# Kernel tuning notes

Measured on AMD Instinct MI355X. Metric: run time of the kernel, lower is better.

Reference implementation:

```python
import jax, jax.numpy as jnp
import numpy as np

B, T, HID = 2, 1024, 768
EXPAND, NH, HD, NG, NS, K = 2, 24, 64, 1, 128, 4
INTER = EXPAND * HID            # 1536
CONV_DIM = INTER + 2 * NG * NS  # 1792
NLVL = 15                       # get_num_levels(16384, base=2)
EPS = 1e-5


def _levels(T):
    # Fenwick-style hierarchical level matrix (HType.WEAK, base 2):
    # level(t, s) = 0 on the diagonal, else msb(t XOR s) + 1.
    t = np.arange(T)
    x = t[:, None] ^ t[None, :]
    lev = np.zeros((T, T), np.int32)
    nz = x > 0
    lev[nz] = np.floor(np.log2(x[nz])).astype(np.int32) + 1
    return lev

_LEV = jnp.asarray(_levels(T))  # [T,T] int32, values in [0, NLVL)


def setup_inputs() -> dict:
    key = jax.random.key(0)
    ks = jax.random.split(key, 4)
    P = INTER + CONV_DIM + NH * (NLVL + 1)  # 3712
    return {
        "hidden_states": jax.random.normal(ks[0], (B, T, HID), jnp.float32),
        "in_proj_w": jax.random.normal(ks[1], (P, HID), jnp.float32) * (HID ** -0.5),
        "conv_w": jax.random.normal(ks[2], (CONV_DIM, 1, K), jnp.float32) * 0.2,
        "conv_b": jnp.zeros((CONV_DIM,), jnp.float32),
        "dt_bias": jnp.ones((NH,), jnp.float32),
        "A_log": jnp.log(jnp.arange(1, NH + 1, dtype=jnp.float32)),
        "L": jnp.ones((NH, NLVL), jnp.float32),
        "D": jnp.ones((NH,), jnp.float32),
        "norm_weight": jnp.ones((INTER,), jnp.float32),
        "out_proj_w": jax.random.normal(ks[3], (HID, INTER), jnp.float32) * (INTER ** -0.5),
    }


def reference(hidden_states, in_proj_w, conv_w, conv_b, dt_bias, A_log, L, D,
              norm_weight, out_proj_w):
    # in_proj and split: [gate | xBC | dt | dl]
    proj = hidden_states @ in_proj_w.T                       # [B,T,P]
    gate = proj[..., :INTER]
    xBC = proj[..., INTER:INTER + CONV_DIM]
    dt = proj[..., INTER + CONV_DIM:INTER + CONV_DIM + NH]
    dl = proj[..., INTER + CONV_DIM + NH:].reshape(B, T, NH, NLVL)

    # fused causal depthwise conv1d + SiLU
    xBC = jax.lax.conv_general_dilated(
        xBC.transpose(0, 2, 1), conv_w, window_strides=(1,),
        padding=[(K - 1, 0)], dimension_numbers=("NCH", "OIH", "NCH"),
        feature_group_count=CONV_DIM) + conv_b[None, :, None]
    xBC = jax.nn.silu(xBC.transpose(0, 2, 1))                # [B,T,CONV_DIM]

    x = xBC[..., :INTER].reshape(B, T, NH, HD)               # [B,T,H,P]
    Bm = xBC[..., INTER:INTER + NG * NS].reshape(B, T, NG, NS)
    Cm = xBC[..., INTER + NG * NS:].reshape(B, T, NG, NS)
    hpg = NH // NG
    Bh = jnp.repeat(Bm, hpg, axis=2)                         # [B,T,H,N]
    Ch = jnp.repeat(Cm, hpg, axis=2)

    dt = jax.nn.softplus(dt + dt_bias)                       # [B,T,H]
    A = -jnp.exp(A_log)                                      # [H]
    cumA = jnp.cumsum(dt * A, axis=1)                        # [B,T,H]

    # semiseparable decay exp(sum_{s<r<=t} dt_r * A), causal-masked
    cA = cumA.transpose(0, 2, 1)                             # [B,H,T]
    diff = cA[:, :, :, None] - cA[:, :, None, :]             # [B,H,T,T]
    mask = jnp.tril(jnp.ones((T, T), bool))
    decay = jnp.exp(jnp.where(mask[None, None], diff, -1e9))

    CB = jnp.einsum("bthn,bshn->bhts", Ch, Bh)               # [B,H,T,T]

    # hierarchical lambda gating: positive lambda, per-head learned scale L
    lam = jax.nn.softplus(dl) * L                            # [B,T,H,NLVL]
    lam_g = jnp.take_along_axis(lam.transpose(0, 2, 1, 3),
                                _LEV[None, None], axis=-1)   # [B,H,T,T]

    M = CB * decay * lam_g * dt.transpose(0, 2, 1)[:, :, None, :]
    y = jnp.einsum("bhts,bshp->bthp", M, x)                  # [B,T,H,P]
    y = y + D[None, None, :, None] * x
    y = y.reshape(B, T, INTER)

    # gated RMSNorm (norm_before_gate=False): norm(y * silu(gate))
    y = y * jax.nn.silu(gate)
    var = jnp.mean(jnp.square(y), axis=-1, keepdims=True)
    y = y * jax.lax.rsqrt(var + EPS) * norm_weight

    return y @ out_proj_w.T                                  # [B,T,HID]
```

## Files before the change

kernel.cpp:

```cpp
#include <hip/hip_runtime.h>
#include <hip/hip_bf16.h>
#include <math.h>

#define B_ 2
#define T_ 1024
#define HID_ 768
#define INTER_ 1536
#define NH_ 24
#define HD_ 64
#define NS_ 128
#define NLVL_ 15
#define CONV_DIM_ 1792
#define P_ 3712
#define EPS_ 1e-5f

typedef short short8_t __attribute__((ext_vector_type(8)));
typedef short short4_t __attribute__((ext_vector_type(4)));
typedef float float4_t __attribute__((ext_vector_type(4)));


__device__ __forceinline__ float softplus_f(float x) {
  return (x > 20.f) ? x : log1pf(__expf(x));
}
__device__ __forceinline__ short f2bf(float f) {
  union { float f; unsigned u; } v; v.f = f;
  unsigned r = v.u + 0x7FFF + ((v.u >> 16) & 1);
  return (short)(r >> 16);
}
__device__ __forceinline__ float bf2f(short s) {
  union { unsigned u; float f; } v; v.u = ((unsigned)(unsigned short)s) << 16;
  return v.f;
}
__device__ __forceinline__ void gl_lds16(const void* g, void* l) {
  __builtin_amdgcn_global_load_lds(
      (const __attribute__((address_space(1))) unsigned int*)g,
      (__attribute__((address_space(3))) unsigned int*)l, 16, 0, 0);
}

__global__ __launch_bounds__(256) void cvtdt_k(
    const float* __restrict__ hs, const float* __restrict__ Win, const float* __restrict__ Wout,
    short* __restrict__ hsbf, short* __restrict__ wibf, short* __restrict__ wobf,
    float* __restrict__ dtraw, int ncvt)
{
  const long na = (long)B_ * T_ * HID_, nb = (long)P_ * HID_, nc = (long)HID_ * INTER_;
  if ((int)blockIdx.x < ncvt) {
    const long i = ((long)blockIdx.x * 256 + threadIdx.x) * 8;
    const float* src; short* dst; long off;
    if (i < na)           { src = hs;   dst = hsbf; off = i; }
    else if (i < na + nb) { src = Win;  dst = wibf; off = i - na; }
    else if (i < na + nb + nc) { src = Wout; dst = wobf; off = i - na - nb; }
    else return;
    const long base = (off & ~31L) + ((off >> 3) & 3) * 4;
    float4 v0 = *(const float4*)(src + base);
    float4 v1 = *(const float4*)(src + base + 16);
    short8_t o;
    o[0] = f2bf(v0.x); o[1] = f2bf(v0.y); o[2] = f2bf(v0.z); o[3] = f2bf(v0.w);
    o[4] = f2bf(v1.x); o[5] = f2bf(v1.y); o[6] = f2bf(v1.z); o[7] = f2bf(v1.w);
    *(short8_t*)(dst + off) = o;
  } else {
    const int rowbt = ((int)blockIdx.x - ncvt) * 4 + (threadIdx.x >> 6);
    const int lane = threadIdx.x & 63;
    float hv[12];
    const float* hrow = hs + (long)rowbt * HID_ + lane * 12;
    #pragma unroll
    for (int j = 0; j < 12; j++) hv[j] = hrow[j];
    const float* wbase = Win + (long)(INTER_ + CONV_DIM_) * HID_ + lane * 12;
    for (int h = 0; h < NH_; h++) {
      const float* wr = wbase + (long)h * HID_;
      float s = 0.f;
      #pragma unroll
      for (int j = 0; j < 12; j++) s = fmaf(hv[j], wr[j], s);
      #pragma unroll
      for (int off = 32; off; off >>= 1) s += __shfl_xor(s, off);
      if (lane == 0) dtraw[(long)rowbt * NH_ + h] = s;
    }
  }
}

__device__ __forceinline__ short8_t ldfrag(const short* Ts, int row, int lg) {
  return *(const short8_t*)(Ts + row * 32 + lg * 8);
}

__device__ __forceinline__ short8_t ldfrag64(const short* Ts, int row, int kk, int lg) {
  const int cc = (kk * 4 + lg) ^ (row & 7);
  return *(const short8_t*)(Ts + row * 64 + cc * 8);
}

__global__ __launch_bounds__(256) void inproj_scan_k(
    const short* __restrict__ A, const short* __restrict__ B, short* __restrict__ C,
    const float* __restrict__ dtraw, const float* __restrict__ dt_bias,
    const float* __restrict__ A_log, float* __restrict__ dtT, float* __restrict__ cAT,
    float* __restrict__ qT)
{
  constexpr int TM = 128, TN = 128, K = HID_, BK = 64;
  constexpr int PSZ = TM * 32;
  constexpr int ASZ = 2 * PSZ;
  __shared__ short As[2 * ASZ];
  __shared__ short Bs[2 * ASZ];

  if (blockIdx.y >= 16) {
    const int sid = ((int)blockIdx.y - 16) * 29 + (int)blockIdx.x;
    if (sid >= B_ * NH_) return;
    const int b = sid / NH_;
    const int h = sid % NH_;
    const float bias = dt_bias[h];
    const float Ah = -__expf(A_log[h]);
    const long ob = (long)(h * B_ + b) * T_;
    float* sc = (float*)As;
    float carry = 0.f;
    for (int c0 = 0; c0 < T_; c0 += 256) {
      const int t = c0 + threadIdx.x;
      const long bt = (long)b * T_ + t;
      float sp = softplus_f(dtraw[bt * NH_ + h] + bias);
      dtT[ob + t] = sp;
      sc[threadIdx.x] = sp * Ah;
      __syncthreads();
      for (int off = 1; off < 256; off <<= 1) {
        float add = (threadIdx.x >= off) ? sc[threadIdx.x - off] : 0.f;
        __syncthreads();
        sc[threadIdx.x] += add;
        __syncthreads();
      }
      cAT[ob + t] = carry + sc[threadIdx.x];
      qT[ob + t] = sp * __expf(sc[threadIdx.x | 63] - sc[threadIdx.x]);
      float tot = sc[255];
      __syncthreads();
      carry += tot;
    }
    return;
  }

  const int tid = threadIdx.x;
  const int w = tid >> 6, lane = tid & 63;
  const int lr = lane & 15, lg = lane >> 4;
  const int wr = w >> 1, wc = w & 1;
  const int m0 = blockIdx.y * TM, n0 = blockIdx.x * TN;
  const int srow = lane >> 2;
  const int sc2 = (lane & 3) * 8;

  auto stage = [&](int buf, int k0) {
    #pragma unroll
    for (int it = 0; it < 2; it++) {
      const int cb = w + 4 * it;
      const int row = cb * 16 + srow;
      #pragma unroll
      for (int kg = 0; kg < 2; kg++) {
        gl_lds16(A + (long)(m0 + row) * K + k0 + kg * 32 + sc2,
                 As + buf * ASZ + kg * PSZ + cb * 512);
        gl_lds16(B + (long)(n0 + row) * K + k0 + kg * 32 + sc2,
                 Bs + buf * ASZ + kg * PSZ + cb * 512);
      }
    }
  };

  float4_t acc[4][4] = {};
  int cur = 0;
  stage(0, 0);
  for (int k0 = 0; k0 < K; k0 += BK) {
    __syncthreads();
    if (k0 + BK < K) stage(cur ^ 1, k0 + BK);
    #pragma unroll
    for (int kg = 0; kg < 2; kg++) {
      const short* Ab = As + cur * ASZ + kg * PSZ;
      const short* Bb = Bs + cur * ASZ + kg * PSZ;
      short8_t af[4], bf[4];
      #pragma unroll
      for (int m = 0; m < 4; m++) af[m] = ldfrag(Ab, wr * 64 + m * 16 + lr, lg);
      #pragma unroll
      for (int n = 0; n < 4; n++) bf[n] = ldfrag(Bb, wc * 64 + n * 16 + lr, lg);
      #pragma unroll
      for (int m = 0; m < 4; m++)
        #pragma unroll
        for (int n = 0; n < 4; n++)
          acc[m][n] = __builtin_amdgcn_mfma_f32_16x16x32_bf16(af[m], bf[n], acc[m][n], 0, 0, 0);
    }
    cur ^= 1;
  }

  #pragma unroll
  for (int m = 0; m < 4; m++)
    #pragma unroll
    for (int n = 0; n < 4; n++)
      #pragma unroll
      for (int r = 0; r < 4; r++) {
        const int row = m0 + wr * 64 + m * 16 + lg * 4 + r;
        const int col = n0 + wc * 64 + n * 16 + lr;
        C[(long)row * P_ + col] = f2bf(acc[m][n][r]);
      }
}

__global__ __launch_bounds__(256) void gemm_out_k(
    const short* __restrict__ A, const short* __restrict__ B, float* __restrict__ C,
    int M, int N, int K)
{
  constexpr int PSZ = 64 * 32;
  constexpr int BKG = 4;
  constexpr int BUF = PSZ * BKG;
  __shared__ short As[2 * BUF];
  __shared__ short Bs[2 * BUF];
  const int tid = threadIdx.x;
  const int w = tid >> 6, lane = tid & 63;
  const int lr = lane & 15, lg = lane >> 4;
  const int wr = w >> 1, wc = w & 1;
  const int m0 = blockIdx.y * 64, n0 = blockIdx.x * 64;
  const int srow = lane >> 2;
  const int sc = (lane & 3) * 8;

  auto stage = [&](int buf, int k0) {
    const int row = w * 16 + srow;
    #pragma unroll
    for (int kg = 0; kg < BKG; kg++) {
      gl_lds16(A + (long)(m0 + row) * K + k0 + kg * 32 + sc, As + buf * BUF + kg * PSZ + w * 512);
      gl_lds16(B + (long)(n0 + row) * K + k0 + kg * 32 + sc, Bs + buf * BUF + kg * PSZ + w * 512);
    }
  };

  float4_t acc[2][2] = {};
  int cur = 0;
  stage(0, 0);
  for (int k0 = 0; k0 < K; k0 += 128) {
    __syncthreads();
    if (k0 + 128 < K) stage(cur ^ 1, k0 + 128);
    #pragma unroll
    for (int kg = 0; kg < BKG; kg++) {
      const short* Ab = As + cur * BUF + kg * PSZ;
      const short* Bb = Bs + cur * BUF + kg * PSZ;
      short8_t af[2], bf[2];
      #pragma unroll
      for (int m = 0; m < 2; m++) af[m] = ldfrag(Ab, wr * 32 + m * 16 + lr, lg);
      #pragma unroll
      for (int n = 0; n < 2; n++) bf[n] = ldfrag(Bb, wc * 32 + n * 16 + lr, lg);
      #pragma unroll
      for (int m = 0; m < 2; m++)
        #pragma unroll
        for (int n = 0; n < 2; n++)
          acc[m][n] = __builtin_amdgcn_mfma_f32_16x16x32_bf16(af[m], bf[n], acc[m][n], 0, 0, 0);
    }
    cur ^= 1;
  }

  #pragma unroll
  for (int m = 0; m < 2; m++)
    #pragma unroll
    for (int n = 0; n < 2; n++)
      #pragma unroll
      for (int r = 0; r < 4; r++) {
        const int row = m0 + wr * 32 + m * 16 + lg * 4 + r;
        const int col = n0 + wc * 32 + n * 16 + lr;
        C[(long)row * N + col] = acc[m][n][r];
      }
}

__global__ __launch_bounds__(256) void gemm_cbh_k(
    const short* __restrict__ Chh, const short* __restrict__ Bh, short* __restrict__ CBh)
{
  if (blockIdx.x > blockIdx.y) return;
  Chh += (long)blockIdx.z * T_ * NS_;
  Bh  += (long)blockIdx.z * T_ * NS_;
  CBh += (long)blockIdx.z * T_ * T_;
  constexpr int PSZ = 64 * 32;
  __shared__ short As[4 * PSZ];
  __shared__ short Bs[4 * PSZ];
  const int tid = threadIdx.x;
  const int w = tid >> 6, lane = tid & 63;
  const int lr = lane & 15, lg = lane >> 4;
  const int wr = w >> 1, wc = w & 1;
  const int m0 = blockIdx.y * 64, n0 = blockIdx.x * 64;
  const int srow = lane >> 2;
  const int sc = (lane & 3) * 8;

  {
    const int row = w * 16 + srow;
    #pragma unroll
    for (int kg = 0; kg < 4; kg++) {
      gl_lds16(Chh + (long)(m0 + row) * NS_ + kg * 32 + sc, As + kg * PSZ + w * 512);
      gl_lds16(Bh  + (long)(n0 + row) * NS_ + kg * 32 + sc, Bs + kg * PSZ + w * 512);
    }
  }
  __syncthreads();

  float4_t acc[2][2] = {};
  #pragma unroll
  for (int kg = 0; kg < 4; kg++) {
    const short* Ab = As + kg * PSZ;
    const short* Bb = Bs + kg * PSZ;
    short8_t af[2], bf[2];
    #pragma unroll
    for (int m = 0; m < 2; m++) af[m] = ldfrag(Ab, wr * 32 + m * 16 + lr, lg);
    #pragma unroll
    for (int n = 0; n < 2; n++) bf[n] = ldfrag(Bb, wc * 32 + n * 16 + lr, lg);
    #pragma unroll
    for (int m = 0; m < 2; m++)
      #pragma unroll
      for (int n = 0; n < 2; n++)
        acc[m][n] = __builtin_amdgcn_mfma_f32_16x16x32_bf16(af[m], bf[n], acc[m][n], 0, 0, 0);
  }

  #pragma unroll
  for (int m = 0; m < 2; m++)
    #pragma unroll
    for (int n = 0; n < 2; n++)
      #pragma unroll
      for (int r = 0; r < 4; r++) {
        const int row = m0 + wr * 32 + m * 16 + lg * 4 + r;
        const int sl = wc * 32 + n * 16 + lr;
        const int g = sl >> 5, k32 = sl & 31;
        const int cc = g * 4 + ((k32 >> 2) & 3);
        const int off = ((cc ^ (row & 7)) * 8) + 4 * (k32 >> 4) + (k32 & 3);
        CBh[(long)row * T_ + n0 + off] = f2bf(acc[m][n][r]);
      }
}

__global__ __launch_bounds__(256) void conv_silu_k(
    const short* __restrict__ projh, const float* __restrict__ cw, const float* __restrict__ cbias,
    const float* __restrict__ qT,
    short* __restrict__ xTr, short* __restrict__ xTq,
    short* __restrict__ Bh, short* __restrict__ Chh)
{
  const int c0 = blockIdx.x * 256;
  const int t0 = blockIdx.y * 16;
  const int b  = blockIdx.z;
  const int tid = threadIdx.x;
  __shared__ float S[19][256];
  for (int q = tid; q < 19 * 32; q += 256) {
    const int r = q >> 5, c8 = (q & 31) * 8;
    const int t = t0 - 3 + r;
    float4 f0 = {0.f, 0.f, 0.f, 0.f}, f1 = {0.f, 0.f, 0.f, 0.f};
    if (t >= 0) {
      short8_t v = *(const short8_t*)(projh + ((long)b * T_ + t) * P_ + INTER_ + c0 + c8);
      f0.x = bf2f(v[0]); f0.y = bf2f(v[1]); f0.z = bf2f(v[2]); f0.w = bf2f(v[3]);
      f1.x = bf2f(v[4]); f1.y = bf2f(v[5]); f1.z = bf2f(v[6]); f1.w = bf2f(v[7]);
    }
    *(float4*)(&S[r][c8])     = f0;
    *(float4*)(&S[r][c8 + 4]) = f1;
  }
  __syncthreads();
  const int c = c0 + tid;
  const float4 w = *(const float4*)(cw + c * 4);
  const float bias = cbias[c];
  float acc[16];
  #pragma unroll
  for (int tt = 0; tt < 16; tt++) {
    float a = bias + w.w * S[tt + 3][tid] + w.z * S[tt + 2][tid]
                   + w.y * S[tt + 1][tid] + w.x * S[tt][tid];
    acc[tt] = a / (1.f + __expf(-a));
  }
  if (c < INTER_) {
    const int h = c >> 6, hd = c & 63;
    const long chb = (long)(h * B_ + b) * T_;
    float qv[16];
    #pragma unroll
    for (int qq = 0; qq < 4; qq++) {
      float4 q4 = *(const float4*)(qT + chb + t0 + qq * 4);
      qv[qq*4+0] = q4.x; qv[qq*4+1] = q4.y; qv[qq*4+2] = q4.z; qv[qq*4+3] = q4.w;
    }
    const long base = ((long)(b * NH_ + h) * HD_ + hd) * T_ + (t0 & ~63);
    const int g = (t0 >> 5) & 1, h2 = (t0 >> 4) & 1, sw = hd & 7;
    #pragma unroll
    for (int a = 0; a < 4; a++) {
      short4_t xr, xq;
      #pragma unroll
      for (int r = 0; r < 4; r++) {
        xr[r] = f2bf(acc[a * 4 + r]);
        xq[r] = f2bf(acc[a * 4 + r] * qv[a * 4 + r]);
      }
      const int off = (((g * 4 + a) ^ sw) * 8) + h2 * 4;
      *(short4_t*)(xTr + base + off) = xr;
      *(short4_t*)(xTq + base + off) = xq;
    }
  } else {
    const int ch0 = c - INTER_;
    const bool isB = ch0 < NS_;
    const int k = isB ? ch0 : ch0 - NS_;
    const int k32 = k & 31;
    const int P = (k & ~31) + 8 * ((k32 >> 2) & 3) + 4 * (k32 >> 4) + (k32 & 3);
    short* dst = isB ? Bh : Chh;
    #pragma unroll
    for (int tt = 0; tt < 16; tt++) {
      const long bt = (long)b * T_ + t0 + tt;
      dst[bt * NS_ + P] = f2bf(acc[tt]);
    }
  }
}

__global__ __launch_bounds__(256) void attn_mfma3_k(
    const short* __restrict__ xTr, const short* __restrict__ xTq,
    const short* __restrict__ CBh,
    const float* __restrict__ cAT, const float* __restrict__ dtT,
    const short* __restrict__ projh, const float* __restrict__ Lw,
    const float* __restrict__ Dv,
    short* __restrict__ ybh)
{
  const int h = blockIdx.x;
  const int tt = (T_ / 64 - 1) - blockIdx.y;
  const int b = blockIdx.z;
  const int t0 = tt * 64;
  const int tid = threadIdx.x;
  const int w = tid >> 6, lane = tid & 63;
  const int lr = lane & 15, lg = lane >> 4;

  __shared__ short CBl[3][64 * 64];
  __shared__ short Xl[3][64 * 64];
  __shared__ float lamS[64][17];
  __shared__ float caEs[16];

  const long chb = (long)(h * B_ + b) * T_;
  for (int f = tid; f < 64 * NLVL_; f += 256) {
    int r = f / NLVL_, l = f - r * NLVL_;
    lamS[r][l] = softplus_f(
        bf2f(projh[((long)b * T_ + t0 + r) * P_ + INTER_ + CONV_DIM_ + NH_ + h * NLVL_ + l]))
        * Lw[h * NLVL_ + l];
  }
  if (tid < 16) caEs[tid] = cAT[chb + tid * 64 + 63];

  const int tl = w * 16 + lr;
  const int t  = t0 + tl;
  const int orow = w * 16 + lg * 4;
  const float catv = cAT[chb + t];
  float cao[4];
  #pragma unroll
  for (int r = 0; r < 4; r++) cao[r] = cAT[chb + t0 + orow + r];

  const short* xbr = xTr + (long)(b * NH_ + h) * HD_ * T_;
  const short* xbq = xTq + (long)(b * NH_ + h) * HD_ * T_;
  const short* CBbase = CBh + (long)b * T_ * T_ + (long)t0 * T_;

  const int srow = w * 16 + (lane >> 3);
  const int sch = (lane & 7) * 8;

  auto stage = [&](int buf, int st) {
    const int s0 = st * 64;
    const short* xsrc = (st == tt) ? xbr : xbq;
    #pragma unroll
    for (int i = 0; i < 2; i++) {
      gl_lds16(CBbase + (long)(srow + i * 8) * T_ + s0 + sch, &CBl[buf][(w * 16 + i * 8) * 64]);
      gl_lds16(xsrc + (long)(srow + i * 8) * T_ + s0 + sch, &Xl[buf][(w * 16 + i * 8) * 64]);
    }
  };

  float4_t acc[4] = {};
  stage(0, 0);
  if (tt >= 1) stage(1, 1);
  asm volatile("s_waitcnt lgkmcnt(0)" ::: "memory");

  for (int st = 0; st <= tt; st++) {
    if (st < tt) asm volatile("s_waitcnt vmcnt(4)" ::: "memory");
    else         asm volatile("s_waitcnt vmcnt(0)" ::: "memory");
    __builtin_amdgcn_s_barrier();
    __builtin_amdgcn_sched_barrier(0);
    if (st + 2 <= tt) stage((st + 2) % 3, st + 2);
    const int cur = st % 3;
    const int s0 = st * 64;
    if (st < tt) {
      const float caE = caEs[st];
      const int lev = 32 - __clz(t0 ^ s0);
      float k1o[4];
      #pragma unroll
      for (int r = 0; r < 4; r++)
        k1o[r] = __expf(cao[r] - caE) * lamS[orow + r][lev];
      float4_t dtile[4] = {};
      __builtin_amdgcn_s_setprio(1);
      #pragma unroll
      for (int kk = 0; kk < 2; kk++) {
        short8_t af = ldfrag64(CBl[cur], tl, kk, lg);
        #pragma unroll
        for (int n = 0; n < 4; n++) {
          short8_t bfv = ldfrag64(Xl[cur], n * 16 + lr, kk, lg);
          dtile[n] = __builtin_amdgcn_mfma_f32_16x16x32_bf16(af, bfv, dtile[n], 0, 0, 0);
        }
      }
      __builtin_amdgcn_s_setprio(0);
      #pragma unroll
      for (int n = 0; n < 4; n++)
        #pragma unroll
        for (int r = 0; r < 4; r++)
          acc[n][r] = fmaf(k1o[r], dtile[n][r], acc[n][r]);
    } else {
      #pragma unroll
      for (int kk = 0; kk < 2; kk++) {
        short8_t cb8 = ldfrag64(CBl[cur], tl, kk, lg);
        short8_t af;
        #pragma unroll
        for (int g = 0; g < 2; g++) {
          const int sb = s0 + kk * 32 + g * 16 + lg * 4;
          float4_t ca4 = *(const float4_t*)(cAT + chb + sb);
          float4_t dt4 = *(const float4_t*)(dtT + chb + sb);
          #pragma unroll
          for (int a = 0; a < 4; a++) {
            const int sg = sb + a;
            float m = 0.f;
            if (sg <= t) {
              const int xo = t ^ sg;
              const int lev2 = xo ? (32 - __clz(xo)) : 0;
              m = bf2f(cb8[g * 4 + a]) * __expf(catv - ca4[a]) * lamS[tl][lev2] * dt4[a];
            }
            af[g * 4 + a] = f2bf(m);
          }
        }
        __builtin_amdgcn_s_setprio(1);
        #pragma unroll
        for (int n = 0; n < 4; n++) {
          short8_t bfv = ldfrag64(Xl[cur], n * 16 + lr, kk, lg);
          acc[n] = __builtin_amdgcn_mfma_f32_16x16x32_bf16(af, bfv, acc[n], 0, 0, 0);
        }
        __builtin_amdgcn_s_setprio(0);
      }
    }
  }

  const float Dh = Dv[h];
  const short* Xd = Xl[tt % 3];
  #pragma unroll
  for (int n = 0; n < 4; n++) {
    #pragma unroll
    for (int r = 0; r < 4; r++) {
      const int trow = t0 + orow + r;
      const int hd = n * 16 + lr;
      const int xoff = hd * 64 + ((((w >> 1) * 4 + lg) ^ (hd & 7)) * 8) + (w & 1) * 4 + r;
      const float xv = bf2f(Xd[xoff]);
      ybh[((long)b * T_ + trow) * INTER_ + h * HD_ + hd] = f2bf(acc[n][r] + Dh * xv);
    }
  }
}

__global__ __launch_bounds__(192) void gate_rms_k(
    const short* __restrict__ ybh, const short* __restrict__ projh,
    const float* __restrict__ nw, short* __restrict__ ynorm)
{
  const long bt = blockIdx.x;
  const short* gp = projh + bt * P_;
  const short* yp = ybh + bt * INTER_;
  const int i = threadIdx.x;
  const int lo = (i >> 2) * 32 + (i & 3) * 4;
  const int hi = lo + 16;
  float v[8];
  float ss = 0.f;
  {
    short4_t g0 = *(const short4_t*)(gp + lo);
    short4_t g1 = *(const short4_t*)(gp + hi);
    short4_t y0 = *(const short4_t*)(yp + lo);
    short4_t y1 = *(const short4_t*)(yp + hi);
    float ga[8] = {bf2f(g0[0]), bf2f(g0[1]), bf2f(g0[2]), bf2f(g0[3]),
                   bf2f(g1[0]), bf2f(g1[1]), bf2f(g1[2]), bf2f(g1[3])};
    float ya[8] = {bf2f(y0[0]), bf2f(y0[1]), bf2f(y0[2]), bf2f(y0[3]),
                   bf2f(y1[0]), bf2f(y1[1]), bf2f(y1[2]), bf2f(y1[3])};
    #pragma unroll
    for (int j = 0; j < 8; j++) {
      float val = ya[j] * (ga[j] / (1.f + __expf(-ga[j])));
      v[j] = val;
      ss += val * val;
    }
  }
  #pragma unroll
  for (int off = 32; off > 0; off >>= 1) ss += __shfl_xor(ss, off);
  __shared__ float part[3];
  if ((i & 63) == 0) part[i >> 6] = ss;
  __syncthreads();
  const float tot = part[0] + part[1] + part[2];
  const float r = rsqrtf(tot * (1.f / INTER_) + EPS_);
  short8_t o;
  #pragma unroll
  for (int j = 0; j < 8; j++) {
    const int idx = (j < 4) ? (lo + j) : (hi + j - 4);
    o[j] = f2bf(v[j] * r * nw[idx]);
  }
  *(short8_t*)(ynorm + bt * INTER_ + i * 8) = o;
}

extern "C" void kernel_launch(void* const* d_in, const int* in_sizes, int n_in,
                              void* d_out, int out_size, void* d_ws, size_t ws_size,
                              hipStream_t stream) {
  const float* hs   = (const float*)d_in[0];
  const float* Win  = (const float*)d_in[1];
  const float* cw   = (const float*)d_in[2];
  const float* cb   = (const float*)d_in[3];
  const float* dtb  = (const float*)d_in[4];
  const float* Alog = (const float*)d_in[5];
  const float* Lw   = (const float*)d_in[6];
  const float* Dv   = (const float*)d_in[7];
  const float* nw   = (const float*)d_in[8];
  const float* Wout = (const float*)d_in[9];
  float* out = (float*)d_out;

  const long n_hs = (long)B_ * T_ * HID_;
  const long n_wi = (long)P_ * HID_;
  const long n_wo = (long)HID_ * INTER_;

  float* ws = (float*)d_ws;
  long o = 0;
  float* projreg = ws + o; o += (long)B_ * T_ * P_ / 2 + 16;
  short* xbf   = (short*)(ws + o); o += (long)B_ * T_ * INTER_ / 2;
  short* Bh    = (short*)(ws + o); o += (long)B_ * T_ * NS_ / 2;
  short* Chh   = (short*)(ws + o); o += (long)B_ * T_ * NS_ / 2;
  float* dtT   = ws + o; o += (long)B_ * T_ * NH_;
  float* cAT   = ws + o; o += (long)B_ * T_ * NH_;
  float* qT    = ws + o; o += (long)B_ * T_ * NH_;
  float* dtraw = ws + o; o += (long)B_ * T_ * NH_;
  short* CBh   = (short*)(ws + o); o += (long)B_ * T_ * T_ / 2;
  short* ybh   = (short*)(ws + o); o += (long)B_ * T_ * INTER_ / 2;
  float* yxreg = ws + o; o += (long)B_ * T_ * INTER_ / 2;
  short* hsbf  = (short*)(ws + o); o += n_hs / 2;
  short* wibf  = (short*)(ws + o); o += n_wi / 2;
  short* wobf  = (short*)(ws + o); o += n_wo / 2;
  short* projh = (short*)projreg;
  short* xTr   = (short*)yxreg;
  short* ynrmb = (short*)yxreg;
  short* xTq   = hsbf;
  (void)xbf;

  const int ncvt = (int)((n_hs + n_wi + n_wo) / 8 / 256);

  cvtdt_k<<<ncvt + (B_ * T_) / 4, 256, 0, stream>>>(
      hs, Win, Wout, hsbf, wibf, wobf, dtraw, ncvt);
  inproj_scan_k<<<dim3(P_ / 128, 18), 256, 0, stream>>>(
      hsbf, wibf, projh, dtraw, dtb, Alog, dtT, cAT, qT);
  conv_silu_k<<<dim3(CONV_DIM_ / 256, T_ / 16, B_), 256, 0, stream>>>(
      projh, cw, cb, qT, xTr, xTq, Bh, Chh);
  gemm_cbh_k<<<dim3(T_ / 64, T_ / 64, B_), 256, 0, stream>>>(Chh, Bh, CBh);
  attn_mfma3_k<<<dim3(NH_, T_ / 64, B_), 256, 0, stream>>>(
      xTr, xTq, CBh, cAT, dtT, projh, Lw, Dv, ybh);
  gate_rms_k<<<B_ * T_, 192, 0, stream>>>(ybh, projh, nw, ynrmb);
  gemm_out_k<<<dim3(HID_ / 64, (B_ * T_) / 64), 256, 0, stream>>>(
      ynrmb, wobf, out, B_ * T_, HID_, INTER_);
}
```

Baseline: 107.4 us.

## Switch in-proj and out-proj GEMMs to three-stage LDS pipeline with partial waitcnt

Both the in-projection GEMM and the output GEMM move from double buffering with a full __syncthreads per K-step to a triple-buffered ring. Each step issues the load two steps ahead and waits with s_waitcnt vmcnt(4), so the newest stage's loads stay in flight. The K-step shrinks (32 for in_proj, 64 for out_proj), which means more barriers but less shared memory per stage. MFMA blocks are also wrapped in s_setprio raises. The risk is that the hand-picked vmcnt value must match the number of outstanding loads per stage.

```diff
diff --git a/kernel.cpp b/kernel.cpp
--- a/kernel.cpp
+++ b/kernel.cpp
@@ -92,11 +92,11 @@
     const float* __restrict__ A_log, float* __restrict__ dtT, float* __restrict__ cAT,
     float* __restrict__ qT)
 {
-  constexpr int TM = 128, TN = 128, K = HID_, BK = 64;
+  constexpr int TM = 128, TN = 128, K = HID_;
   constexpr int PSZ = TM * 32;
-  constexpr int ASZ = 2 * PSZ;
-  __shared__ short As[2 * ASZ];
-  __shared__ short Bs[2 * ASZ];
+  constexpr int NSTEP = K / 32;
+  __shared__ short As[3 * PSZ];
+  __shared__ short Bs[3 * PSZ];
 
   if (blockIdx.y >= 16) {
     const int sid = ((int)blockIdx.y - 16) * 29 + (int)blockIdx.x;
@@ -143,38 +143,34 @@
     for (int it = 0; it < 2; it++) {
       const int cb = w + 4 * it;
       const int row = cb * 16 + srow;
-      #pragma unroll
-      for (int kg = 0; kg < 2; kg++) {
-        gl_lds16(A + (long)(m0 + row) * K + k0 + kg * 32 + sc2,
-                 As + buf * ASZ + kg * PSZ + cb * 512);
-        gl_lds16(B + (long)(n0 + row) * K + k0 + kg * 32 + sc2,
-                 Bs + buf * ASZ + kg * PSZ + cb * 512);
-      }
+      gl_lds16(A + (long)(m0 + row) * K + k0 + sc2, As + buf * PSZ + cb * 512);
+      gl_lds16(B + (long)(n0 + row) * K + k0 + sc2, Bs + buf * PSZ + cb * 512);
     }
   };
 
   float4_t acc[4][4] = {};
-  int cur = 0;
   stage(0, 0);
-  for (int k0 = 0; k0 < K; k0 += BK) {
-    __syncthreads();
-    if (k0 + BK < K) stage(cur ^ 1, k0 + BK);
-    #pragma unroll
-    for (int kg = 0; kg < 2; kg++) {
-      const short* Ab = As + cur * ASZ + kg * PSZ;
-      const short* Bb = Bs + cur * ASZ + kg * PSZ;
-      short8_t af[4], bf[4];
-      #pragma unroll
-      for (int m = 0; m < 4; m++) af[m] = ldfrag(Ab, wr * 64 + m * 16 + lr, lg);
-      #pragma unroll
-      for (int n = 0; n < 4; n++) bf[n] = ldfrag(Bb, wc * 64 + n * 16 + lr, lg);
-      #pragma unroll
-      for (int m = 0; m < 4; m++)
-        #pragma unroll
-        for (int n = 0; n < 4; n++)
-          acc[m][n] = __builtin_amdgcn_mfma_f32_16x16x32_bf16(af[m], bf[n], acc[m][n], 0, 0, 0);
-    }
-    cur ^= 1;
+  stage(1, 32);
+  for (int ks = 0; ks < NSTEP; ks++) {
+    if (ks < NSTEP - 1) asm volatile("s_waitcnt vmcnt(4)" ::: "memory");
+    else                asm volatile("s_waitcnt vmcnt(0)" ::: "memory");
+    __builtin_amdgcn_s_barrier();
+    __builtin_amdgcn_sched_barrier(0);
+    if (ks + 2 < NSTEP) stage((ks + 2) % 3, (ks + 2) * 32);
+    const short* Ab = As + (ks % 3) * PSZ;
+    const short* Bb = Bs + (ks % 3) * PSZ;
+    short8_t af[4], bf[4];
+    #pragma unroll
+    for (int m = 0; m < 4; m++) af[m] = ldfrag(Ab, wr * 64 + m * 16 + lr, lg);
+    #pragma unroll
+    for (int n = 0; n < 4; n++) bf[n] = ldfrag(Bb, wc * 64 + n * 16 + lr, lg);
+    __builtin_amdgcn_s_setprio(1);
+    #pragma unroll
+    for (int m = 0; m < 4; m++)
+      #pragma unroll
+      for (int n = 0; n < 4; n++)
+        acc[m][n] = __builtin_amdgcn_mfma_f32_16x16x32_bf16(af[m], bf[n], acc[m][n], 0, 0, 0);
+    __builtin_amdgcn_s_setprio(0);
   }
 
   #pragma unroll
@@ -194,10 +190,10 @@
     int M, int N, int K)
 {
   constexpr int PSZ = 64 * 32;
-  constexpr int BKG = 4;
+  constexpr int BKG = 2;
   constexpr int BUF = PSZ * BKG;
-  __shared__ short As[2 * BUF];
-  __shared__ short Bs[2 * BUF];
+  __shared__ short As[3 * BUF];
+  __shared__ short Bs[3 * BUF];
   const int tid = threadIdx.x;
   const int w = tid >> 6, lane = tid & 63;
   const int lr = lane & 15, lg = lane >> 4;
@@ -205,6 +201,7 @@
   const int m0 = blockIdx.y * 64, n0 = blockIdx.x * 64;
   const int srow = lane >> 2;
   const int sc = (lane & 3) * 8;
+  const int NSTEP = K / 64;
 
   auto stage = [&](int buf, int k0) {
     const int row = w * 16 + srow;
@@ -216,27 +213,31 @@
   };
 
   float4_t acc[2][2] = {};
-  int cur = 0;
   stage(0, 0);
-  for (int k0 = 0; k0 < K; k0 += 128) {
-    __syncthreads();
-    if (k0 + 128 < K) stage(cur ^ 1, k0 + 128);
+  stage(1, 64);
+  for (int ks = 0; ks < NSTEP; ks++) {
+    if (ks < NSTEP - 1) asm volatile("s_waitcnt vmcnt(4)" ::: "memory");
+    else                asm volatile("s_waitcnt vmcnt(0)" ::: "memory");
+    __builtin_amdgcn_s_barrier();
+    __builtin_amdgcn_sched_barrier(0);
+    if (ks + 2 < NSTEP) stage((ks + 2) % 3, (ks + 2) * 64);
     #pragma unroll
     for (int kg = 0; kg < BKG; kg++) {
-      const short* Ab = As + cur * BUF + kg * PSZ;
-      const short* Bb = Bs + cur * BUF + kg * PSZ;
+      const short* Ab = As + (ks % 3) * BUF + kg * PSZ;
+      const short* Bb = Bs + (ks % 3) * BUF + kg * PSZ;
       short8_t af[2], bf[2];
       #pragma unroll
       for (int m = 0; m < 2; m++) af[m] = ldfrag(Ab, wr * 32 + m * 16 + lr, lg);
       #pragma unroll
       for (int n = 0; n < 2; n++) bf[n] = ldfrag(Bb, wc * 32 + n * 16 + lr, lg);
+      __builtin_amdgcn_s_setprio(1);
       #pragma unroll
       for (int m = 0; m < 2; m++)
         #pragma unroll
         for (int n = 0; n < 2; n++)
           acc[m][n] = __builtin_amdgcn_mfma_f32_16x16x32_bf16(af[m], bf[n], acc[m][n], 0, 0, 0);
-    }
-    cur ^= 1;
+      __builtin_amdgcn_s_setprio(0);
+    }
   }
 
   #pragma unroll
```

Measured after the change: 112.6 us. 4.8% more time.

## Process two heads per attention block to reuse the shared CB tile

Applied to the files above, without the earlier changes.

Each attention workgroup now handles two heads instead of one. The CB tile is shared across heads because NG=1, so each CB tile staged into LDS serves twice the MFMA work, halving global CB traffic. The lambda table is transposed to a level-major layout. The trade-off is half as many workgroups, more LDS (extra X buffers) and more accumulator registers, which may lower occupancy and parallelism.

```diff
diff --git a/kernel.cpp b/kernel.cpp
--- a/kernel.cpp
+++ b/kernel.cpp
@@ -391,7 +391,7 @@
     const float* __restrict__ Dv,
     short* __restrict__ ybh)
 {
-  const int h = blockIdx.x;
+  const int h0 = blockIdx.x * 2;
   const int tt = (T_ / 64 - 1) - blockIdx.y;
   const int b = blockIdx.z;
   const int t0 = tt * 64;
@@ -400,29 +400,39 @@
   const int lr = lane & 15, lg = lane >> 4;
 
   __shared__ short CBl[3][64 * 64];
-  __shared__ short Xl[3][64 * 64];
-  __shared__ float lamS[64][17];
-  __shared__ float caEs[16];
-
-  const long chb = (long)(h * B_ + b) * T_;
-  for (int f = tid; f < 64 * NLVL_; f += 256) {
-    int r = f / NLVL_, l = f - r * NLVL_;
-    lamS[r][l] = softplus_f(
-        bf2f(projh[((long)b * T_ + t0 + r) * P_ + INTER_ + CONV_DIM_ + NH_ + h * NLVL_ + l]))
-        * Lw[h * NLVL_ + l];
-  }
-  if (tid < 16) caEs[tid] = cAT[chb + tid * 64 + 63];
+  __shared__ short Xl[2][3][64 * 64];
+  __shared__ float lamS[2][NLVL_ * 64];
+  __shared__ float caEs[2][16];
+
+  #pragma unroll 1
+  for (int f = tid; f < 2 * 64 * NLVL_; f += 256) {
+    const int hh = f / (64 * NLVL_);
+    const int rem = f - hh * 64 * NLVL_;
+    const int r = rem / NLVL_, l = rem - r * NLVL_;
+    lamS[hh][l * 64 + r] = softplus_f(
+        bf2f(projh[((long)b * T_ + t0 + r) * P_ + INTER_ + CONV_DIM_ + NH_ + (h0 + hh) * NLVL_ + l]))
+        * Lw[(h0 + hh) * NLVL_ + l];
+  }
+  if (tid < 32)
+    caEs[tid >> 4][tid & 15] =
+        cAT[(long)((h0 + (tid >> 4)) * B_ + b) * T_ + (tid & 15) * 64 + 63];
 
   const int tl = w * 16 + lr;
   const int t  = t0 + tl;
   const int orow = w * 16 + lg * 4;
-  const float catv = cAT[chb + t];
-  float cao[4];
-  #pragma unroll
-  for (int r = 0; r < 4; r++) cao[r] = cAT[chb + t0 + orow + r];
-
-  const short* xbr = xTr + (long)(b * NH_ + h) * HD_ * T_;
-  const short* xbq = xTq + (long)(b * NH_ + h) * HD_ * T_;
+
+  long chb[2]; float catv[2]; float cao[2][4];
+  const short *xbr[2], *xbq[2];
+  #pragma unroll
+  for (int hh = 0; hh < 2; hh++) {
+    const int h = h0 + hh;
+    chb[hh] = (long)(h * B_ + b) * T_;
+    catv[hh] = cAT[chb[hh] + t];
+    #pragma unroll
+    for (int r = 0; r < 4; r++) cao[hh][r] = cAT[chb[hh] + t0 + orow + r];
+    xbr[hh] = xTr + (long)(b * NH_ + h) * HD_ * T_;
+    xbq[hh] = xTq + (long)(b * NH_ + h) * HD_ * T_;
+  }
   const short* CBbase = CBh + (long)b * T_ * T_ + (long)t0 * T_;
 
   const int srow = w * 16 + (lane >> 3);
@@ -430,21 +440,25 @@
 
   auto stage = [&](int buf, int st) {
     const int s0 = st * 64;
-    const short* xsrc = (st == tt) ? xbr : xbq;
-    #pragma unroll
-    for (int i = 0; i < 2; i++) {
+    #pragma unroll
+    for (int i = 0; i < 2; i++)
       gl_lds16(CBbase + (long)(srow + i * 8) * T_ + s0 + sch, &CBl[buf][(w * 16 + i * 8) * 64]);
-      gl_lds16(xsrc + (long)(srow + i * 8) * T_ + s0 + sch, &Xl[buf][(w * 16 + i * 8) * 64]);
+    #pragma unroll
+    for (int hh = 0; hh < 2; hh++) {
+      const short* xsrc = (st == tt) ? xbr[hh] : xbq[hh];
+      #pragma unroll
+      for (int i = 0; i < 2; i++)
+        gl_lds16(xsrc + (long)(srow + i * 8) * T_ + s0 + sch, &Xl[hh][buf][(w * 16 + i * 8) * 64]);
     }
   };
 
-  float4_t acc[4] = {};
+  float4_t acc[2][4] = {};
   stage(0, 0);
   if (tt >= 1) stage(1, 1);
   asm volatile("s_waitcnt lgkmcnt(0)" ::: "memory");
 
   for (int st = 0; st <= tt; st++) {
-    if (st < tt) asm volatile("s_waitcnt vmcnt(4)" ::: "memory");
+    if (st < tt) asm volatile("s_waitcnt vmcnt(6)" ::: "memory");
     else         asm volatile("s_waitcnt vmcnt(0)" ::: "memory");
     __builtin_amdgcn_s_barrier();
     __builtin_amdgcn_sched_barrier(0);
@@ -452,73 +466,82 @@
     const int cur = st % 3;
     const int s0 = st * 64;
     if (st < tt) {
-      const float caE = caEs[st];
       const int lev = 32 - __clz(t0 ^ s0);
-      float k1o[4];
-      #pragma unroll
-      for (int r = 0; r < 4; r++)
-        k1o[r] = __expf(cao[r] - caE) * lamS[orow + r][lev];
-      float4_t dtile[4] = {};
-      __builtin_amdgcn_s_setprio(1);
-      #pragma unroll
-      for (int kk = 0; kk < 2; kk++) {
-        short8_t af = ldfrag64(CBl[cur], tl, kk, lg);
-        #pragma unroll
-        for (int n = 0; n < 4; n++) {
-          short8_t bfv = ldfrag64(Xl[cur], n * 16 + lr, kk, lg);
-          dtile[n] = __builtin_amdgcn_mfma_f32_16x16x32_bf16(af, bfv, dtile[n], 0, 0, 0);
-        }
-      }
-      __builtin_amdgcn_s_setprio(0);
-      #pragma unroll
-      for (int n = 0; n < 4; n++)
+      #pragma unroll
+      for (int hh = 0; hh < 2; hh++) {
+        const float caE = caEs[hh][st];
+        float k1o[4];
         #pragma unroll
         for (int r = 0; r < 4; r++)
-          acc[n][r] = fmaf(k1o[r], dtile[n][r], acc[n][r]);
+          k1o[r] = __expf(cao[hh][r] - caE) * lamS[hh][lev * 64 + orow + r];
+        float4_t dtile[4] = {};
+        __builtin_amdgcn_s_setprio(1);
+        #pragma unroll
+        for (int kk = 0; kk < 2; kk++) {
+          short8_t af = ldfrag64(CBl[cur], tl, kk, lg);
+          #pragma unroll
+          for (int n = 0; n < 4; n++) {
+            short8_t bfv = ldfrag64(Xl[hh][cur], n * 16 + lr, kk, lg);
+            dtile[n] = __builtin_amdgcn_mfma_f32_16x16x32_bf16(af, bfv, dtile[n], 0, 0, 0);
+          }
+        }
+        __builtin_amdgcn_s_setprio(0);
+        #pragma unroll
+        for (int n = 0; n < 4; n++)
+          #pragma unroll
+          for (int r = 0; r < 4; r++)
+            acc[hh][n][r] = fmaf(k1o[r], dtile[n][r], acc[hh][n][r]);
+      }
     } else {
       #pragma unroll
       for (int kk = 0; kk < 2; kk++) {
         short8_t cb8 = ldfrag64(CBl[cur], tl, kk, lg);
-        short8_t af;
         #pragma unroll
-        for (int g = 0; g < 2; g++) {
-          const int sb = s0 + kk * 32 + g * 16 + lg * 4;
-          float4_t ca4 = *(const float4_t*)(cAT + chb + sb);
-          float4_t dt4 = *(const float4_t*)(dtT + chb + sb);
+        for (int hh = 0; hh < 2; hh++) {
+          short8_t af;
           #pragma unroll
-          for (int a = 0; a < 4; a++) {
-            const int sg = sb + a;
-            float m = 0.f;
-            if (sg <= t) {
-              const int xo = t ^ sg;
-              const int lev2 = xo ? (32 - __clz(xo)) : 0;
-              m = bf2f(cb8[g * 4 + a]) * __expf(catv - ca4[a]) * lamS[tl][lev2] * dt4[a];
+          for (int g = 0; g < 2; g++) {
+            const int sb = s0 + kk * 32 + g * 16 + lg * 4;
+            float4_t ca4 = *(const float4_t*)(cAT + chb[hh] + sb);
+            float4_t dt4 = *(const float4_t*)(dtT + chb[hh] + sb);
+            #pragma unroll
+            for (int a = 0; a < 4; a++) {
+              const int sg = sb + a;
+              float m = 0.f;
+              if (sg <= t) {
+                const int xo = t ^ sg;
+                const int lev2 = xo ? (32 - __clz(xo)) : 0;
+                m = bf2f(cb8[g * 4 + a]) * __expf(catv[hh] - ca4[a]) * lamS[hh][lev2 * 64 + tl] * dt4[a];
+              }
+              af[g * 4 + a] = f2bf(m);
             }
-            af[g * 4 + a] = f2bf(m);
           }
+          __builtin_amdgcn_s_setprio(1);
+          #pragma unroll
+          for (int n = 0; n < 4; n++) {
+            short8_t bfv = ldfrag64(Xl[hh][cur], n * 16 + lr, kk, lg);
+            acc[hh][n] = __builtin_amdgcn_mfma_f32_16x16x32_bf16(af, bfv, acc[hh][n], 0, 0, 0);
+          }
+          __builtin_amdgcn_s_setprio(0);
         }
-        __builtin_amdgcn_s_setprio(1);
-        #pragma unroll
-        for (int n = 0; n < 4; n++) {
-          short8_t bfv = ldfrag64(Xl[cur], n * 16 + lr, kk, lg);
-          acc[n] = __builtin_amdgcn_mfma_f32_16x16x32_bf16(af, bfv, acc[n], 0, 0, 0);
-        }
-        __builtin_amdgcn_s_setprio(0);
-      }
-    }
-  }
-
-  const float Dh = Dv[h];
-  const short* Xd = Xl[tt % 3];
-  #pragma unroll
-  for (int n = 0; n < 4; n++) {
-    #pragma unroll
-    for (int r = 0; r < 4; r++) {
-      const int trow = t0 + orow + r;
-      const int hd = n * 16 + lr;
-      const int xoff = hd * 64 + ((((w >> 1) * 4 + lg) ^ (hd & 7)) * 8) + (w & 1) * 4 + r;
-      const float xv = bf2f(Xd[xoff]);
-      ybh[((long)b * T_ + trow) * INTER_ + h * HD_ + hd] = f2bf(acc[n][r] + Dh * xv);
+      }
+    }
+  }
+
+  #pragma unroll
+  for (int hh = 0; hh < 2; hh++) {
+    const float Dh = Dv[h0 + hh];
+    const short* Xd = Xl[hh][tt % 3];
+    #pragma unroll
+    for (int n = 0; n < 4; n++) {
+      #pragma unroll
+      for (int r = 0; r < 4; r++) {
+        const int trow = t0 + orow + r;
+        const int hd = n * 16 + lr;
+        const int xoff = hd * 64 + ((((w >> 1) * 4 + lg) ^ (hd & 7)) * 8) + (w & 1) * 4 + r;
+        const float xv = bf2f(Xd[xoff]);
+        ybh[((long)b * T_ + trow) * INTER_ + (h0 + hh) * HD_ + hd] = f2bf(acc[hh][n][r] + Dh * xv);
+      }
     }
   }
 }
@@ -617,7 +640,7 @@
   conv_silu_k<<<dim3(CONV_DIM_ / 256, T_ / 16, B_), 256, 0, stream>>>(
       projh, cw, cb, qT, xTr, xTq, Bh, Chh);
   gemm_cbh_k<<<dim3(T_ / 64, T_ / 64, B_), 256, 0, stream>>>(Chh, Bh, CBh);
-  attn_mfma3_k<<<dim3(NH_, T_ / 64, B_), 256, 0, stream>>>(
+  attn_mfma3_k<<<dim3(NH_ / 2, T_ / 64, B_), 256, 0, stream>>>(
       xTr, xTq, CBh, cAT, dtT, projh, Lw, Dv, ybh);
   gate_rms_k<<<B_ * T_, 192, 0, stream>>>(ybh, projh, nw, ynrmb);
   gemm_out_k<<<dim3(HID_ / 64, (B_ * T_) / 64), 256, 0, stream>>>(
```

New measurement: 119.8 us. 1.12x slower.
